# Performance work log

Measured on AMD Instinct MI355X. Metric: run time of the kernel, lower is better.

The kernel has to match this reference:

```python
import jax, jax.numpy as jnp
import numpy as np

D_MODEL = 512
N_HEADS = 8
D_K = D_MODEL // N_HEADS
LN_EPS = 1e-5


def setup_inputs() -> dict:
    key = jax.random.key(0)
    ks = jax.random.split(key, 8)
    B, S, D = 2, 4096, D_MODEL
    # xavier_uniform bound for square [D, D] weight
    bound = float(np.sqrt(6.0 / (D + D)))
    x = jax.random.normal(ks[0], (B, S, D), dtype=jnp.float32)
    w_q = jax.random.uniform(ks[1], (D, D), jnp.float32, -bound, bound)
    w_k = jax.random.uniform(ks[2], (D, D), jnp.float32, -bound, bound)
    w_v = jax.random.uniform(ks[3], (D, D), jnp.float32, -bound, bound)
    # w_o: torch Linear default init (kaiming-uniform-ish); uniform is fine as data
    lim = float(1.0 / np.sqrt(D))
    w_o = jax.random.uniform(ks[4], (D, D), jnp.float32, -lim, lim)
    b_o = jax.random.uniform(ks[5], (D,), jnp.float32, -lim, lim)
    ln_gamma = jnp.ones((D,), jnp.float32)
    ln_beta = jnp.zeros((D,), jnp.float32)
    return {"x": x, "w_q": w_q, "w_k": w_k, "w_v": w_v,
            "w_o": w_o, "b_o": b_o, "ln_gamma": ln_gamma, "ln_beta": ln_beta}


def _layer_norm(x, gamma, beta):
    mu = jnp.mean(x, axis=-1, keepdims=True)
    var = jnp.mean(jnp.square(x - mu), axis=-1, keepdims=True)
    return (x - mu) * jax.lax.rsqrt(var + LN_EPS) * gamma + beta


def reference(x, w_q, w_k, w_v, w_o, b_o, ln_gamma, ln_beta):
    B, S, D = x.shape
    residual = x
    h = _layer_norm(x, ln_gamma, ln_beta)
    # torch Linear: y = h @ W.T ; reshape to [B, H, S, d_k]
    def proj(W):
        return (h @ W.T).reshape(B, S, N_HEADS, D_K).transpose(0, 2, 1, 3)
    Q, K, V = proj(w_q), proj(w_k), proj(w_v)
    scores = jnp.einsum('bhqd,bhkd->bhqk', Q, K) / jnp.sqrt(jnp.float32(D_K))
    attn = jax.nn.softmax(scores, axis=-1)  # dropout p=0 -> identity
    attended = jnp.einsum('bhqk,bhkd->bhqd', attn, V)
    attended = attended.transpose(0, 2, 1, 3).reshape(B, S, D)
    out = attended @ w_o.T + b_o
    return out + residual
```

## Files before the change

kernel.cpp:

```cpp
#include <hip/hip_runtime.h>
#include <hip/hip_bf16.h>
#include <stdint.h>


typedef __bf16 bf16;
typedef __attribute__((ext_vector_type(8))) __bf16 bf16x8;
typedef __attribute__((ext_vector_type(4))) __bf16 bf16x4;
typedef __attribute__((ext_vector_type(4))) float f32x4;
typedef __attribute__((ext_vector_type(4))) unsigned int u32x4;

#define LOG2E 1.44269504088896340736f
#define SW(row, grp) (((row) << 6) + ((((grp) ^ ((row) & 7))) << 3))

__device__ __forceinline__ unsigned int pkbf16(float lo, float hi) {
  return __builtin_amdgcn_perm(__builtin_bit_cast(unsigned int, hi),
                               __builtin_bit_cast(unsigned int, lo),
                               0x07060302u);
}

__device__ __forceinline__ void gl_lds16(const bf16* g, bf16* l) {
  __builtin_amdgcn_global_load_lds(
      (const __attribute__((address_space(1))) void*)g,
      (__attribute__((address_space(3))) void*)l, 16, 0, 0);
}

__global__ __launch_bounds__(256) void ln_kernel(
    const float* __restrict__ x, const float* __restrict__ gamma,
    const float* __restrict__ beta, bf16* __restrict__ h) {
  int wave = threadIdx.x >> 6, lane = threadIdx.x & 63;
  int row = blockIdx.x * 4 + wave;
  const float* xr = x + (size_t)row * 512 + lane * 8;
  f32x4 v0 = *(const f32x4*)xr;
  f32x4 v1 = *(const f32x4*)(xr + 4);
  float f[8], s = 0.f, s2 = 0.f;
#pragma unroll
  for (int i = 0; i < 4; ++i) { f[i] = v0[i]; f[4 + i] = v1[i]; }
#pragma unroll
  for (int i = 0; i < 8; ++i) { s += f[i]; s2 += f[i] * f[i]; }
#pragma unroll
  for (int off = 1; off < 64; off <<= 1) {
    s  += __shfl_xor(s, off, 64);
    s2 += __shfl_xor(s2, off, 64);
  }
  float mu  = s * (1.f / 512.f);
  float var = s2 * (1.f / 512.f) - mu * mu;
  float rstd = rsqrtf(var + 1e-5f);
  f32x4 g0 = *(const f32x4*)(gamma + lane * 8);
  f32x4 g1 = *(const f32x4*)(gamma + lane * 8 + 4);
  f32x4 b0 = *(const f32x4*)(beta + lane * 8);
  f32x4 b1 = *(const f32x4*)(beta + lane * 8 + 4);
  bf16x8 o;
#pragma unroll
  for (int i = 0; i < 4; ++i) {
    o[i]     = (bf16)((f[i]     - mu) * rstd * g0[i] + b0[i]);
    o[4 + i] = (bf16)((f[4 + i] - mu) * rstd * g1[i] + b1[i]);
  }
  *(bf16x8*)(h + (size_t)row * 512 + lane * 8) = o;
}

__global__ __launch_bounds__(256) void qkv_kernel(
    const bf16* __restrict__ h, const float* __restrict__ wq,
    const float* __restrict__ wk, const float* __restrict__ wv,
    bf16* __restrict__ Qg, bf16* __restrict__ Kg, bf16* __restrict__ Vtg) {
  __shared__ bf16 smemq[2 * 128 * 64];
  bf16* As = smemq;
  bf16* Bs = smemq + 128 * 64;
  int tid = threadIdx.x, wave = tid >> 6, lane = tid & 63;
  int wm = wave >> 1, wn = wave & 1, quad = lane >> 4, l15 = lane & 15;
  int lin = blockIdx.x + (blockIdx.y << 6);
  int xcd = lin & 7, idx = lin >> 3;
  int mtile = xcd * 8 + idx / 12;
  int yy = idx % 12;
  int wsel = yy >> 2;
  int nb = yy & 3;
  const float* W = (wsel == 0) ? wq : (wsel == 1 ? wk : wv);
  const bf16*  Abase = h + (size_t)mtile * 128 * 512;
  const float* Bbase = W + (size_t)nb * 128 * 512;
  f32x4 acc[4][4];
#pragma unroll
  for (int i = 0; i < 4; ++i)
#pragma unroll
    for (int j = 0; j < 4; ++j) acc[i][j] = (f32x4){0.f, 0.f, 0.f, 0.f};

  int srow = tid >> 3, grp = tid & 7, scol = grp * 8;
  bf16x8 ar[4];
  f32x4 br0[4], br1[4];
#pragma unroll
  for (int k = 0; k < 4; ++k) {
    int rr = srow + k * 32;
    ar[k]  = *(const bf16x8*)(Abase + (size_t)rr * 512 + scol);
    br0[k] = *(const f32x4*)(Bbase + (size_t)rr * 512 + scol);
    br1[k] = *(const f32x4*)(Bbase + (size_t)rr * 512 + scol + 4);
  }
  for (int k0 = 0; k0 < 512; k0 += 64) {
#pragma unroll
    for (int k = 0; k < 4; ++k) {
      int rr = srow + k * 32;
      int w = SW(rr, grp);
      *(bf16x8*)(As + w) = ar[k];
      bf16x8 wb;
#pragma unroll
      for (int j = 0; j < 4; ++j) { wb[j] = (bf16)br0[k][j]; wb[4 + j] = (bf16)br1[k][j]; }
      *(bf16x8*)(Bs + w) = wb;
    }
    __syncthreads();
    if (k0 < 448) {
#pragma unroll
      for (int k = 0; k < 4; ++k) {
        int rr = srow + k * 32;
        ar[k]  = *(const bf16x8*)(Abase + (size_t)rr * 512 + k0 + 64 + scol);
        br0[k] = *(const f32x4*)(Bbase + (size_t)rr * 512 + k0 + 64 + scol);
        br1[k] = *(const f32x4*)(Bbase + (size_t)rr * 512 + k0 + 64 + scol + 4);
      }
    }
#pragma unroll
    for (int c = 0; c < 2; ++c) {
      bf16x8 af[4], bw[4];
#pragma unroll
      for (int mt = 0; mt < 4; ++mt)
        af[mt] = *(const bf16x8*)(As + SW(wm * 64 + mt * 16 + l15, c * 4 + quad));
#pragma unroll
      for (int nt = 0; nt < 4; ++nt)
        bw[nt] = *(const bf16x8*)(Bs + SW(wn * 64 + nt * 16 + l15, c * 4 + quad));
#pragma unroll
      for (int mt = 0; mt < 4; ++mt)
#pragma unroll
        for (int nt = 0; nt < 4; ++nt)
          acc[mt][nt] = __builtin_amdgcn_mfma_f32_16x16x32_bf16(
              bw[nt], af[mt], acc[mt][nt], 0, 0, 0);
    }
    __syncthreads();
  }
  if (wsel < 2) {
    float qscale = (wsel == 0) ? (0.125f * LOG2E) : 1.0f;
#pragma unroll
    for (int mt = 0; mt < 4; ++mt) {
      int m_g = mtile * 128 + wm * 64 + mt * 16 + l15;
      int b = m_g >> 12, s = m_g & 4095;
#pragma unroll
      for (int nt = 0; nt < 4; ++nt) {
        int n_g = nb * 128 + wn * 64 + nt * 16 + quad * 4;
        int head = n_g >> 6, d = n_g & 63;
        f32x4 a = acc[mt][nt];
        bf16* dst = (wsel == 0 ? Qg : Kg) +
                    ((size_t)((b * 8 + head) * 4096 + s)) * 64 + d;
        bf16x4 pk;
#pragma unroll
        for (int r = 0; r < 4; ++r) pk[r] = (bf16)(a[r] * qscale);
        *(bf16x4*)dst = pk;
      }
    }
  } else {
    bf16* Vt = smemq;
#pragma unroll
    for (int mt = 0; mt < 4; ++mt) {
      int t = wm * 64 + mt * 16 + l15;
#pragma unroll
      for (int nt = 0; nt < 4; ++nt) {
#pragma unroll
        for (int r = 0; r < 4; ++r) {
          int f = wn * 64 + nt * 16 + quad * 4 + r;
          Vt[f * 128 + (t ^ ((f & 7) << 3))] = (bf16)acc[mt][nt][r];
        }
      }
    }
    __syncthreads();
    int fr = tid >> 1, hf = tid & 1;
    int n_g = nb * 128 + fr;
    int head = n_g >> 6, d = n_g & 63;
    int bb = mtile >> 5;
    bf16* dst = Vtg + ((size_t)((bb * 8 + head) * 64 + d)) * 4096 +
                (mtile & 31) * 128 + hf * 64;
    int sx3 = (fr & 7) << 3;
#pragma unroll
    for (int g = 0; g < 8; ++g) {
      int pr = g >> 2, qd = g & 3;
      int tb = hf * 64 + pr * 32 + qd * 4;
      bf16x4 lo  = *(const bf16x4*)(Vt + fr * 128 + (tb ^ sx3));
      bf16x4 hi4 = *(const bf16x4*)(Vt + fr * 128 + ((tb + 16) ^ sx3));
      bf16x8 v;
#pragma unroll
      for (int j = 0; j < 4; ++j) { v[j] = lo[j]; v[4 + j] = hi4[j]; }
      *(bf16x8*)(dst + g * 8) = v;
    }
  }
}

__global__ __launch_bounds__(256, 2) void attn_kernel(
    const bf16* __restrict__ Qg, const bf16* __restrict__ Kg,
    const bf16* __restrict__ Vtg, bf16* __restrict__ Og) {
  __shared__ char smem[64 * 1024];
  bf16* KV = (bf16*)smem;
  float* OL = (float*)smem;
  float* Ll = (float*)(smem + 49152);

  int tid = threadIdx.x, wave = tid >> 6, lane = tid & 63;
  int quad = lane >> 4, l15 = lane & 15;
  int qgrp = wave & 1, khalf = wave >> 1;
  int lin = blockIdx.x;
  int bh = ((lin & 7) << 1) | ((lin >> 3) & 1);
  int q0 = (lin >> 4) * 128;
  int hi = bh & 7, bi = bh >> 3;
  const bf16* Kh  = Kg  + (size_t)bh * 4096 * 64;
  const bf16* Vth = Vtg + (size_t)bh * 64 * 4096;

  bf16x8 qf[4][2];
#pragma unroll
  for (int mt = 0; mt < 4; ++mt)
#pragma unroll
    for (int c = 0; c < 2; ++c)
      qf[mt][c] = *(const bf16x8*)(
          Qg + ((size_t)bh * 4096 + q0 + qgrp * 64 + mt * 16 + l15) * 64 +
          c * 32 + quad * 8);

  f32x4 o_acc[4][4], lacc[4];
#pragma unroll
  for (int mt = 0; mt < 4; ++mt) {
    lacc[mt] = (f32x4){0.f, 0.f, 0.f, 0.f};
#pragma unroll
    for (int nt = 0; nt < 4; ++nt) o_acc[mt][nt] = (f32x4){0.f, 0.f, 0.f, 0.f};
  }
  const u32x4 onesu = {0x3F803F80u, 0x3F803F80u, 0x3F803F80u, 0x3F803F80u};
  const bf16x8 ones8 = __builtin_bit_cast(bf16x8, onesu);
  const f32x4 z4 = {0.f, 0.f, 0.f, 0.f};

  int key0 = khalf * 2048;
  int lr = lane >> 3, lg = (lane & 7) ^ (lr & 7);
  const bf16* gKb = Kh + ((size_t)key0 + lr) * 64 + lg * 8;
  const bf16* gVb = Vth + (size_t)lr * 4096 + key0 + lg * 8;
  bf16* myK = KV + khalf * 8192;
  bf16* myV = myK + 4096;

  if (qgrp == 0) {
#pragma unroll
    for (int i = 0; i < 8; ++i) gl_lds16(gKb + i * 512, myK + i * 512);
  } else {
#pragma unroll
    for (int i = 0; i < 8; ++i)
      gl_lds16(gVb + (size_t)i * 32768, myV + i * 512);
  }
  __syncthreads();

  for (int kt = 0; kt < 32; ++kt) {
    int cur = kt & 1, nxt = cur ^ 1;
    bf16* Ksw = KV + cur * 16384 + khalf * 8192;
    bf16* Vsw = Ksw + 4096;
    if (kt < 31) {
      if (qgrp == 0) {
        const bf16* src = gKb + (size_t)(kt + 1) * 4096;
        bf16* d = myK + nxt * 16384;
#pragma unroll
        for (int i = 0; i < 8; ++i) gl_lds16(src + i * 512, d + i * 512);
      } else {
        const bf16* src = gVb + (kt + 1) * 64;
        bf16* d = myV + nxt * 16384;
#pragma unroll
        for (int i = 0; i < 8; ++i)
          gl_lds16(src + (size_t)i * 32768, d + i * 512);
      }
    }
    bf16x8 kf[8];
#pragma unroll
    for (int kb = 0; kb < 4; ++kb)
#pragma unroll
      for (int c = 0; c < 2; ++c)
        kf[kb * 2 + c] = *(const bf16x8*)(Ksw + SW(kb * 16 + l15, c * 4 + quad));
    bf16x8 vf8[2][4];
#pragma unroll
    for (int pr = 0; pr < 2; ++pr)
#pragma unroll
      for (int nt = 0; nt < 4; ++nt)
        vf8[pr][nt] = *(const bf16x8*)(Vsw + SW(nt * 16 + l15, pr * 4 + quad));
#pragma unroll
    for (int mt = 0; mt < 4; ++mt) {
      f32x4 st[4];
#pragma unroll
      for (int kb = 0; kb < 4; ++kb)
        st[kb] = __builtin_amdgcn_mfma_f32_16x16x32_bf16(
            kf[kb * 2], qf[mt][0], z4, 0, 0, 0);
#pragma unroll
      for (int kb = 0; kb < 4; ++kb)
        st[kb] = __builtin_amdgcn_mfma_f32_16x16x32_bf16(
            kf[kb * 2 + 1], qf[mt][1], st[kb], 0, 0, 0);
#pragma unroll
      for (int pr = 0; pr < 2; ++pr) {
        float ea[4], eb[4];
#pragma unroll
        for (int r = 0; r < 4; ++r) {
          ea[r] = __builtin_amdgcn_exp2f(st[pr * 2][r]);
          eb[r] = __builtin_amdgcn_exp2f(st[pr * 2 + 1][r]);
        }
        u32x4 pw = {pkbf16(ea[0], ea[1]), pkbf16(ea[2], ea[3]),
                    pkbf16(eb[0], eb[1]), pkbf16(eb[2], eb[3])};
        bf16x8 pk8 = __builtin_bit_cast(bf16x8, pw);
#pragma unroll
        for (int nt = 0; nt < 4; ++nt)
          o_acc[mt][nt] = __builtin_amdgcn_mfma_f32_16x16x32_bf16(
              vf8[pr][nt], pk8, o_acc[mt][nt], 0, 0, 0);
        lacc[mt] = __builtin_amdgcn_mfma_f32_16x16x32_bf16(
            ones8, pk8, lacc[mt], 0, 0, 0);
      }
    }
    __syncthreads();
  }
  if (khalf == 1) {
    float* dst = OL + qgrp * 4096;
#pragma unroll
    for (int mt = 0; mt < 4; ++mt) {
#pragma unroll
      for (int nt = 0; nt < 4; ++nt) {
        int row = mt * 16 + l15;
        int g = nt * 4 + quad;
        int gs = (g & 8) | ((g ^ row) & 7);
        *(f32x4*)(&dst[row * 64 + gs * 4]) = o_acc[mt][nt];
      }
      if (quad == 0) Ll[qgrp * 64 + mt * 16 + l15] = lacc[mt][0];
    }
  }
  __syncthreads();
  if (khalf == 0) {
    const float* src = OL + qgrp * 4096;
#pragma unroll
    for (int mt = 0; mt < 4; ++mt) {
      float lt = lacc[mt][0] + Ll[qgrp * 64 + mt * 16 + l15];
      float inv = 1.0f / lt;
      int q = q0 + qgrp * 64 + mt * 16 + l15;
#pragma unroll
      for (int nt = 0; nt < 4; ++nt) {
        int row = mt * 16 + l15;
        int g = nt * 4 + quad;
        int gs = (g & 8) | ((g ^ row) & 7);
        f32x4 o = *(const f32x4*)(&src[row * 64 + gs * 4]);
        bf16x4 pk;
#pragma unroll
        for (int r = 0; r < 4; ++r)
          pk[r] = (bf16)((o[r] + o_acc[mt][nt][r]) * inv);
        *(bf16x4*)(&Og[((size_t)bi * 4096 + q) * 512 + hi * 64 + nt * 16 +
                       quad * 4]) = pk;
      }
    }
  }
}

__global__ __launch_bounds__(256) void proj_kernel(
    const bf16* __restrict__ A, const float* __restrict__ Wo,
    const float* __restrict__ bo, const float* __restrict__ x,
    float* __restrict__ out) {
  __shared__ bf16 As[128 * 64];
  __shared__ bf16 Bs[128 * 64];
  int tid = threadIdx.x, wave = tid >> 6, lane = tid & 63;
  int wm = wave >> 1, wn = wave & 1, quad = lane >> 4, l15 = lane & 15;
  int mtile = blockIdx.x, nb = blockIdx.y;
  const bf16*  Abase = A + (size_t)mtile * 128 * 512;
  const float* Bbase = Wo + (size_t)nb * 128 * 512;
  f32x4 acc[4][4];
#pragma unroll
  for (int i = 0; i < 4; ++i)
#pragma unroll
    for (int j = 0; j < 4; ++j) acc[i][j] = (f32x4){0.f, 0.f, 0.f, 0.f};

  int srow = tid >> 3, grp = tid & 7, scol = grp * 8;
  bf16x8 ar[4];
  f32x4 br0[4], br1[4];
#pragma unroll
  for (int k = 0; k < 4; ++k) {
    int rr = srow + k * 32;
    ar[k]  = *(const bf16x8*)(Abase + (size_t)rr * 512 + scol);
    br0[k] = *(const f32x4*)(Bbase + (size_t)rr * 512 + scol);
    br1[k] = *(const f32x4*)(Bbase + (size_t)rr * 512 + scol + 4);
  }
  for (int k0 = 0; k0 < 512; k0 += 64) {
#pragma unroll
    for (int k = 0; k < 4; ++k) {
      int rr = srow + k * 32;
      int w = SW(rr, grp);
      *(bf16x8*)(As + w) = ar[k];
      bf16x8 wb;
#pragma unroll
      for (int j = 0; j < 4; ++j) { wb[j] = (bf16)br0[k][j]; wb[4 + j] = (bf16)br1[k][j]; }
      *(bf16x8*)(Bs + w) = wb;
    }
    __syncthreads();
    if (k0 < 448) {
#pragma unroll
      for (int k = 0; k < 4; ++k) {
        int rr = srow + k * 32;
        ar[k]  = *(const bf16x8*)(Abase + (size_t)rr * 512 + k0 + 64 + scol);
        br0[k] = *(const f32x4*)(Bbase + (size_t)rr * 512 + k0 + 64 + scol);
        br1[k] = *(const f32x4*)(Bbase + (size_t)rr * 512 + k0 + 64 + scol + 4);
      }
    }
#pragma unroll
    for (int c = 0; c < 2; ++c) {
      bf16x8 af[4], bw[4];
#pragma unroll
      for (int mt = 0; mt < 4; ++mt)
        af[mt] = *(const bf16x8*)(As + SW(wm * 64 + mt * 16 + l15, c * 4 + quad));
#pragma unroll
      for (int nt = 0; nt < 4; ++nt)
        bw[nt] = *(const bf16x8*)(Bs + SW(wn * 64 + nt * 16 + l15, c * 4 + quad));
#pragma unroll
      for (int mt = 0; mt < 4; ++mt)
#pragma unroll
        for (int nt = 0; nt < 4; ++nt)
          acc[mt][nt] = __builtin_amdgcn_mfma_f32_16x16x32_bf16(
              bw[nt], af[mt], acc[mt][nt], 0, 0, 0);
    }
    __syncthreads();
  }
#pragma unroll
  for (int mt = 0; mt < 4; ++mt) {
    int m_g = mtile * 128 + wm * 64 + mt * 16 + l15;
#pragma unroll
    for (int nt = 0; nt < 4; ++nt) {
      int n_g = nb * 128 + wn * 64 + nt * 16 + quad * 4;
      f32x4 a = acc[mt][nt];
      f32x4 xr = *(const f32x4*)(x + (size_t)m_g * 512 + n_g);
      f32x4 bb = *(const f32x4*)(bo + n_g);
      f32x4 o;
#pragma unroll
      for (int r = 0; r < 4; ++r)
        o[r] = a[r] + bb[r] + xr[r];
      *(f32x4*)(out + (size_t)m_g * 512 + n_g) = o;
    }
  }
}

extern "C" void kernel_launch(void* const* d_in, const int* in_sizes, int n_in,
                              void* d_out, int out_size, void* d_ws, size_t ws_size,
                              hipStream_t stream) {
  const float* x     = (const float*)d_in[0];
  const float* wq    = (const float*)d_in[1];
  const float* wk    = (const float*)d_in[2];
  const float* wv    = (const float*)d_in[3];
  const float* wo    = (const float*)d_in[4];
  const float* bo    = (const float*)d_in[5];
  const float* gamma = (const float*)d_in[6];
  const float* beta  = (const float*)d_in[7];
  float* out = (float*)d_out;
  char* ws = (char*)d_ws;
  const size_t SZ = (size_t)8192 * 512 * sizeof(bf16);
  bf16* h   = (bf16*)(ws);
  bf16* Ao  = (bf16*)(ws);
  bf16* Qg  = (bf16*)(ws + SZ);
  bf16* Kg  = (bf16*)(ws + 2 * SZ);
  bf16* Vtg = (bf16*)(ws + 3 * SZ);

  ln_kernel<<<2048, 256, 0, stream>>>(x, gamma, beta, h);
  qkv_kernel<<<dim3(64, 12), 256, 0, stream>>>(h, wq, wk, wv, Qg, Kg, Vtg);
  attn_kernel<<<512, 256, 0, stream>>>(Qg, Kg, Vtg, Ao);
  proj_kernel<<<dim3(64, 4), 256, 0, stream>>>(Ao, wo, bo, x, out);
}
```

Before: 185.6 us.

## Pre-convert weights to bf16 in LN kernel and use async LDS loads in GEMMs

```diff
diff --git a/kernel.cpp b/kernel.cpp
--- a/kernel.cpp
+++ b/kernel.cpp
@@ -26,7 +26,23 @@
 
 __global__ __launch_bounds__(256) void ln_kernel(
     const float* __restrict__ x, const float* __restrict__ gamma,
-    const float* __restrict__ beta, bf16* __restrict__ h) {
+    const float* __restrict__ beta, bf16* __restrict__ h,
+    const float* __restrict__ wq, const float* __restrict__ wk,
+    const float* __restrict__ wv, const float* __restrict__ wo,
+    bf16* __restrict__ wb) {
+  if (blockIdx.x >= 2048) {
+    int cblk = blockIdx.x - 2048;
+    int m = cblk >> 7;
+    int off = (cblk & 127) * 2048 + threadIdx.x * 8;
+    const float* src = (m == 0 ? wq : m == 1 ? wk : m == 2 ? wv : wo) + off;
+    f32x4 a = *(const f32x4*)src;
+    f32x4 b = *(const f32x4*)(src + 4);
+    bf16x8 o;
+#pragma unroll
+    for (int j = 0; j < 4; ++j) { o[j] = (bf16)a[j]; o[4 + j] = (bf16)b[j]; }
+    *(bf16x8*)(wb + (size_t)m * 262144 + off) = o;
+    return;
+  }
   int wave = threadIdx.x >> 6, lane = threadIdx.x & 63;
   int row = blockIdx.x * 4 + wave;
   const float* xr = x + (size_t)row * 512 + lane * 8;
@@ -59,12 +75,9 @@
 }
 
 __global__ __launch_bounds__(256) void qkv_kernel(
-    const bf16* __restrict__ h, const float* __restrict__ wq,
-    const float* __restrict__ wk, const float* __restrict__ wv,
+    const bf16* __restrict__ h, const bf16* __restrict__ wb,
     bf16* __restrict__ Qg, bf16* __restrict__ Kg, bf16* __restrict__ Vtg) {
-  __shared__ bf16 smemq[2 * 128 * 64];
-  bf16* As = smemq;
-  bf16* Bs = smemq + 128 * 64;
+  __shared__ bf16 smemq[2 * 2 * 8192];
   int tid = threadIdx.x, wave = tid >> 6, lane = tid & 63;
   int wm = wave >> 1, wn = wave & 1, quad = lane >> 4, l15 = lane & 15;
   int lin = blockIdx.x + (blockIdx.y << 6);
@@ -73,44 +86,42 @@
   int yy = idx % 12;
   int wsel = yy >> 2;
   int nb = yy & 3;
-  const float* W = (wsel == 0) ? wq : (wsel == 1 ? wk : wv);
-  const bf16*  Abase = h + (size_t)mtile * 128 * 512;
-  const float* Bbase = W + (size_t)nb * 128 * 512;
+  const bf16* Abase = h + (size_t)mtile * 128 * 512;
+  const bf16* Bbase = wb + (size_t)wsel * 262144 + (size_t)nb * 128 * 512;
   f32x4 acc[4][4];
 #pragma unroll
   for (int i = 0; i < 4; ++i)
 #pragma unroll
     for (int j = 0; j < 4; ++j) acc[i][j] = (f32x4){0.f, 0.f, 0.f, 0.f};
 
-  int srow = tid >> 3, grp = tid & 7, scol = grp * 8;
-  bf16x8 ar[4];
-  f32x4 br0[4], br1[4];
-#pragma unroll
-  for (int k = 0; k < 4; ++k) {
-    int rr = srow + k * 32;
-    ar[k]  = *(const bf16x8*)(Abase + (size_t)rr * 512 + scol);
-    br0[k] = *(const f32x4*)(Bbase + (size_t)rr * 512 + scol);
-    br1[k] = *(const f32x4*)(Bbase + (size_t)rr * 512 + scol + 4);
-  }
-  for (int k0 = 0; k0 < 512; k0 += 64) {
-#pragma unroll
-    for (int k = 0; k < 4; ++k) {
-      int rr = srow + k * 32;
-      int w = SW(rr, grp);
-      *(bf16x8*)(As + w) = ar[k];
-      bf16x8 wb;
-#pragma unroll
-      for (int j = 0; j < 4; ++j) { wb[j] = (bf16)br0[k][j]; wb[4 + j] = (bf16)br1[k][j]; }
-      *(bf16x8*)(Bs + w) = wb;
-    }
-    __syncthreads();
-    if (k0 < 448) {
-#pragma unroll
-      for (int k = 0; k < 4; ++k) {
-        int rr = srow + k * 32;
-        ar[k]  = *(const bf16x8*)(Abase + (size_t)rr * 512 + k0 + 64 + scol);
-        br0[k] = *(const f32x4*)(Bbase + (size_t)rr * 512 + k0 + 64 + scol);
-        br1[k] = *(const f32x4*)(Bbase + (size_t)rr * 512 + k0 + 64 + scol + 4);
+  int g0 = wave * 2048 + lane * 8;
+  int srcOff[4];
+#pragma unroll
+  for (int i = 0; i < 4; ++i) {
+    int g = g0 + i * 512;
+    int lr = g >> 6, lg = ((g >> 3) & 7) ^ (lr & 7);
+    srcOff[i] = lr * 512 + lg * 8;
+  }
+  int dstOff = wave * 2048;
+
+#pragma unroll
+  for (int i = 0; i < 4; ++i) {
+    gl_lds16(Abase + srcOff[i], smemq + dstOff + i * 512);
+    gl_lds16(Bbase + srcOff[i], smemq + 8192 + dstOff + i * 512);
+  }
+  __syncthreads();
+
+  for (int kt = 0; kt < 8; ++kt) {
+    int cur = kt & 1;
+    bf16* As = smemq + cur * 16384;
+    bf16* Bs = As + 8192;
+    if (kt < 7) {
+      int nxt = cur ^ 1, k0n = (kt + 1) * 64;
+      bf16* An = smemq + nxt * 16384;
+#pragma unroll
+      for (int i = 0; i < 4; ++i) {
+        gl_lds16(Abase + k0n + srcOff[i], An + dstOff + i * 512);
+        gl_lds16(Bbase + k0n + srcOff[i], An + 8192 + dstOff + i * 512);
       }
     }
 #pragma unroll
@@ -343,51 +354,49 @@
 }
 
 __global__ __launch_bounds__(256) void proj_kernel(
-    const bf16* __restrict__ A, const float* __restrict__ Wo,
+    const bf16* __restrict__ A, const bf16* __restrict__ wo_b,
     const float* __restrict__ bo, const float* __restrict__ x,
     float* __restrict__ out) {
-  __shared__ bf16 As[128 * 64];
-  __shared__ bf16 Bs[128 * 64];
+  __shared__ bf16 smemq[2 * 2 * 8192];
   int tid = threadIdx.x, wave = tid >> 6, lane = tid & 63;
   int wm = wave >> 1, wn = wave & 1, quad = lane >> 4, l15 = lane & 15;
   int mtile = blockIdx.x, nb = blockIdx.y;
-  const bf16*  Abase = A + (size_t)mtile * 128 * 512;
-  const float* Bbase = Wo + (size_t)nb * 128 * 512;
+  const bf16* Abase = A + (size_t)mtile * 128 * 512;
+  const bf16* Bbase = wo_b + (size_t)nb * 128 * 512;
   f32x4 acc[4][4];
 #pragma unroll
   for (int i = 0; i < 4; ++i)
 #pragma unroll
     for (int j = 0; j < 4; ++j) acc[i][j] = (f32x4){0.f, 0.f, 0.f, 0.f};
 
-  int srow = tid >> 3, grp = tid & 7, scol = grp * 8;
-  bf16x8 ar[4];
-  f32x4 br0[4], br1[4];
-#pragma unroll
-  for (int k = 0; k < 4; ++k) {
-    int rr = srow + k * 32;
-    ar[k]  = *(const bf16x8*)(Abase + (size_t)rr * 512 + scol);
-    br0[k] = *(const f32x4*)(Bbase + (size_t)rr * 512 + scol);
-    br1[k] = *(const f32x4*)(Bbase + (size_t)rr * 512 + scol + 4);
-  }
-  for (int k0 = 0; k0 < 512; k0 += 64) {
-#pragma unroll
-    for (int k = 0; k < 4; ++k) {
-      int rr = srow + k * 32;
-      int w = SW(rr, grp);
-      *(bf16x8*)(As + w) = ar[k];
-      bf16x8 wb;
-#pragma unroll
-      for (int j = 0; j < 4; ++j) { wb[j] = (bf16)br0[k][j]; wb[4 + j] = (bf16)br1[k][j]; }
-      *(bf16x8*)(Bs + w) = wb;
-    }
-    __syncthreads();
-    if (k0 < 448) {
-#pragma unroll
-      for (int k = 0; k < 4; ++k) {
-        int rr = srow + k * 32;
-        ar[k]  = *(const bf16x8*)(Abase + (size_t)rr * 512 + k0 + 64 + scol);
-        br0[k] = *(const f32x4*)(Bbase + (size_t)rr * 512 + k0 + 64 + scol);
-        br1[k] = *(const f32x4*)(Bbase + (size_t)rr * 512 + k0 + 64 + scol + 4);
+  int g0 = wave * 2048 + lane * 8;
+  int srcOff[4];
+#pragma unroll
+  for (int i = 0; i < 4; ++i) {
+    int g = g0 + i * 512;
+    int lr = g >> 6, lg = ((g >> 3) & 7) ^ (lr & 7);
+    srcOff[i] = lr * 512 + lg * 8;
+  }
+  int dstOff = wave * 2048;
+
+#pragma unroll
+  for (int i = 0; i < 4; ++i) {
+    gl_lds16(Abase + srcOff[i], smemq + dstOff + i * 512);
+    gl_lds16(Bbase + srcOff[i], smemq + 8192 + dstOff + i * 512);
+  }
+  __syncthreads();
+
+  for (int kt = 0; kt < 8; ++kt) {
+    int cur = kt & 1;
+    bf16* As = smemq + cur * 16384;
+    bf16* Bs = As + 8192;
+    if (kt < 7) {
+      int nxt = cur ^ 1, k0n = (kt + 1) * 64;
+      bf16* An = smemq + nxt * 16384;
+#pragma unroll
+      for (int i = 0; i < 4; ++i) {
+        gl_lds16(Abase + k0n + srcOff[i], An + dstOff + i * 512);
+        gl_lds16(Bbase + k0n + srcOff[i], An + 8192 + dstOff + i * 512);
       }
     }
 #pragma unroll
@@ -445,9 +454,10 @@
   bf16* Qg  = (bf16*)(ws + SZ);
   bf16* Kg  = (bf16*)(ws + 2 * SZ);
   bf16* Vtg = (bf16*)(ws + 3 * SZ);
-
-  ln_kernel<<<2048, 256, 0, stream>>>(x, gamma, beta, h);
-  qkv_kernel<<<dim3(64, 12), 256, 0, stream>>>(h, wq, wk, wv, Qg, Kg, Vtg);
+  bf16* wb  = (bf16*)(ws + 4 * SZ);
+
+  ln_kernel<<<2560, 256, 0, stream>>>(x, gamma, beta, h, wq, wk, wv, wo, wb);
+  qkv_kernel<<<dim3(64, 12), 256, 0, stream>>>(h, wb, Qg, Kg, Vtg);
   attn_kernel<<<512, 256, 0, stream>>>(Qg, Kg, Vtg, Ao);
-  proj_kernel<<<dim3(64, 4), 256, 0, stream>>>(Ao, wo, bo, x, out);
-}
+  proj_kernel<<<dim3(64, 4), 256, 0, stream>>>(Ao, wb + 3 * 262144, bo, x, out);
+}
```

New measurement: 176.6 us. 4.8% less time.
